# Kernel tuning notes

Measured on AMD Instinct MI355X. Metric: run time of the kernel, lower is better.

Reference implementation:

```python
import jax, jax.numpy as jnp
import numpy as np


def setup_inputs() -> dict:
    key = jax.random.key(0)
    x = jax.random.normal(key, (8192, 4096), dtype=jnp.float32)
    return {"x": x, "p": 64}


def reference(x, p):
    # training-mode path: find top-p indices per row (descending sort, first p)
    # and overwrite those positions with -1000. mask = ones, so mask*x == x.
    _, idx = jax.lax.top_k(x, p)                      # [B, p] int32
    rows = jnp.arange(x.shape[0])[:, None]            # [B, 1]
    out = x.at[rows, idx].set(jnp.float32(-1000.0))
    return out
```

## Files before the change

kernel.cpp:

```cpp
#include <hip/hip_runtime.h>
#include <stdint.h>

#define COLS 4096
#define NEGV (-1000.0f)

__device__ __forceinline__ uint32_t f2key(float f) {
    uint32_t u = __float_as_uint(f);
    return u ^ (uint32_t)(((int32_t)u >> 31) | (int32_t)0x80000000);
}
__device__ __forceinline__ float key2f(uint32_t k) {
    uint32_t u = (k & 0x80000000u) ? (k ^ 0x80000000u) : ~k;
    return __uint_as_float(u);
}

template <int PER>
__device__ __forceinline__ void find_bin(const uint32_t* hist, int t, int lane, int wave,
                                         uint32_t rem, uint32_t* s_wsum,
                                         volatile uint32_t* s_dig, volatile uint32_t* s_rem) {
    const int base = t * PER;
    uint32_t own[PER];
    uint32_t L = 0;
#pragma unroll
    for (int i = 0; i < PER; ++i) { own[i] = hist[base + i]; L += own[i]; }
    uint32_t inc = L;
#pragma unroll
    for (int d = 1; d < 64; d <<= 1) {
        uint32_t tmp = (uint32_t)__shfl_down((int)inc, d, 64);
        if (lane + d < 64) inc += tmp;
    }
    if (lane == 0) s_wsum[wave] = inc;
    __syncthreads();
    uint32_t U = inc - L;
#pragma unroll
    for (int w = 1; w < 4; ++w) if (wave + w < 4) U += s_wsum[wave + w];
    uint32_t acc = U;
#pragma unroll
    for (int i = PER - 1; i >= 0; --i) {
        uint32_t h = own[i];
        if (h != 0u && acc < rem && rem <= acc + h) {
            *s_dig = (uint32_t)(base + i);
            *s_rem = rem - acc;
        }
        acc += h;
    }
    __syncthreads();
}

extern "C" __global__ __launch_bounds__(256, 8)
void intent_dropout_kernel(const float* __restrict__ x,
                           const int* __restrict__ pp,
                           float* __restrict__ out) {
    __shared__ uint32_t s_h1[2048];
    __shared__ uint32_t s_h2[2048];
    __shared__ uint32_t s_grpmax[64];
    __shared__ uint32_t s_wsum[4];
    __shared__ uint32_t s_Ckey;
    __shared__ uint32_t s_dig, s_remv;
    __shared__ uint32_t s_eqcnt;

    const int row  = blockIdx.x;
    const int t    = threadIdx.x;
    const int lane = t & 63;
    const int wave = t >> 6;
    const uint32_t P = (uint32_t)pp[0];

    const float4* xr   = (const float4*)(x + (size_t)row * COLS);
    float4*       orow = (float4*)(out + (size_t)row * COLS);

    uint32_t keys[16];
#pragma unroll
    for (int j = 0; j < 4; ++j) {
        float4 v = xr[t + 256 * j];
        keys[4 * j + 0] = f2key(v.x);
        keys[4 * j + 1] = f2key(v.y);
        keys[4 * j + 2] = f2key(v.z);
        keys[4 * j + 3] = f2key(v.w);
    }
#pragma unroll
    for (int i = 0; i < 8; ++i) { s_h1[t + 256 * i] = 0u; s_h2[t + 256 * i] = 0u; }
    if (t == 0) s_eqcnt = 0u;

#pragma unroll
    for (int j = 0; j < 4; ++j) {
        uint32_t m = max(max(keys[4 * j], keys[4 * j + 1]), max(keys[4 * j + 2], keys[4 * j + 3]));
#pragma unroll
        for (int d = 1; d < 16; d <<= 1) m = max(m, (uint32_t)__shfl_xor((int)m, d, 64));
        if ((lane & 15) == 0) s_grpmax[(t >> 4) + 16 * j] = m;
    }
    __syncthreads();

    if (t < 64) {
        uint32_t g = s_grpmax[t];
#pragma unroll
        for (int d = 1; d < 64; d <<= 1) g = min(g, (uint32_t)__shfl_xor((int)g, d, 64));
        if (t == 0) s_Ckey = g;
    }
    __syncthreads();
    const uint32_t Ckey = s_Ckey;

#pragma unroll
    for (int i = 0; i < 16; ++i)
        if (keys[i] >= Ckey) atomicAdd(&s_h1[keys[i] >> 21], 1u);
    __syncthreads();
    find_bin<8>(s_h1, t, lane, wave, P, s_wsum, &s_dig, &s_remv);
    const uint32_t d1   = s_dig;
    const uint32_t rem1 = s_remv;

#pragma unroll
    for (int i = 0; i < 4; ++i) s_h1[t + 256 * i] = 0u;
#pragma unroll
    for (int i = 0; i < 16; ++i)
        if (keys[i] >= Ckey && (keys[i] >> 21) == d1)
            atomicAdd(&s_h2[(keys[i] >> 10) & 0x7FFu], 1u);
    __syncthreads();
    find_bin<8>(s_h2, t, lane, wave, rem1, s_wsum, &s_dig, &s_remv);
    const uint32_t d2   = s_dig;
    const uint32_t rem2 = s_remv;
    const uint32_t pre21 = (d1 << 11) | d2;

#pragma unroll
    for (int i = 0; i < 16; ++i)
        if (keys[i] >= Ckey && (keys[i] >> 10) == pre21)
            atomicAdd(&s_h1[keys[i] & 0x3FFu], 1u);
    __syncthreads();
    find_bin<4>(s_h1, t, lane, wave, rem2, s_wsum, &s_dig, &s_remv);
    const uint32_t Tkey = (pre21 << 10) | s_dig;
    const uint32_t keq  = s_remv;

#pragma unroll
    for (int j = 0; j < 4; ++j) {
#pragma unroll
        for (int c = 0; c < 4; ++c) {
            if (keys[4 * j + c] == Tkey) {
                uint32_t s = atomicAdd(&s_eqcnt, 1u);
                if (s < 2048u) s_h2[s] = (uint32_t)(4 * t + 1024 * j + c);
            }
        }
    }
    __syncthreads();
    const uint32_t eqc = (s_eqcnt < 2048u) ? s_eqcnt : 2048u;

#pragma unroll
    for (int j = 0; j < 4; ++j) {
        float4 o;
        float* comp = (float*)&o;
#pragma unroll
        for (int c = 0; c < 4; ++c) {
            uint32_t k = keys[4 * j + c];
            float f;
            if (k > Tkey) {
                f = NEGV;
            } else if (k == Tkey) {
                uint32_t myi = (uint32_t)(4 * t + 1024 * j + c);
                uint32_t r = 0;
                for (uint32_t e = 0; e < eqc; ++e) r += (uint32_t)(s_h2[e] < myi);
                f = (r < keq) ? NEGV : key2f(k);
            } else {
                f = key2f(k);
            }
            comp[c] = f;
        }
        orow[t + 256 * j] = o;
    }
}

extern "C" void kernel_launch(void* const* d_in, const int* in_sizes, int n_in,
                              void* d_out, int out_size, void* d_ws, size_t ws_size,
                              hipStream_t stream) {
    const float* x   = (const float*)d_in[0];
    const int*   pp  = (const int*)d_in[1];
    float*       out = (float*)d_out;
    int rows = in_sizes[0] / COLS;
    hipLaunchKernelGGL(intent_dropout_kernel, dim3(rows), dim3(256), 0, stream,
                       x, pp, out);
}
```

Baseline: 231.0 us.

## Replace later radix passes with small candidate-list rank selection and halve block size

Cuts the block to 128 threads, each holding 32 keys, which lowers LDS use (one histogram plus small candidate buffers) to allow more resident blocks. After the first 11-bit histogram pass, keys in the selected bin are compacted into a 128-entry candidate list and ranked by brute-force pairwise comparison to find the exact threshold key and cut index. The later radix passes run only when the list overflows, and exact ties fall back to an index histogram. This removes two histogram passes and the per-element tie-rank loop in the common case, at the cost of more register pressure and a more complex fallback path.

After: 261.9 us. +13.3%, slower.

```diff
diff --git a/kernel.cpp b/kernel.cpp
--- a/kernel.cpp
+++ b/kernel.cpp
@@ -2,6 +2,9 @@
 #include <stdint.h>
 
 #define COLS 4096
+#define TPB  128
+#define F4PT 8
+#define CAP  128
 #define NEGV (-1000.0f)
 
 __device__ __forceinline__ uint32_t f2key(float f) {
@@ -15,11 +18,10 @@
 
 template <int PER>
 __device__ __forceinline__ void find_bin(const uint32_t* hist, int t, int lane, int wave,
-                                         uint32_t rem, uint32_t* s_wsum,
+                                         uint32_t rem, volatile uint32_t* s_wsum,
                                          volatile uint32_t* s_dig, volatile uint32_t* s_rem) {
     const int base = t * PER;
-    uint32_t own[PER];
-    uint32_t L = 0;
+    uint32_t own[PER]; uint32_t L = 0;
 #pragma unroll
     for (int i = 0; i < PER; ++i) { own[i] = hist[base + i]; L += own[i]; }
     uint32_t inc = L;
@@ -31,32 +33,26 @@
     if (lane == 0) s_wsum[wave] = inc;
     __syncthreads();
     uint32_t U = inc - L;
-#pragma unroll
-    for (int w = 1; w < 4; ++w) if (wave + w < 4) U += s_wsum[wave + w];
+    if (wave == 0) U += s_wsum[1];
     uint32_t acc = U;
 #pragma unroll
     for (int i = PER - 1; i >= 0; --i) {
         uint32_t h = own[i];
-        if (h != 0u && acc < rem && rem <= acc + h) {
-            *s_dig = (uint32_t)(base + i);
-            *s_rem = rem - acc;
-        }
+        if (h && acc < rem && rem <= acc + h) { *s_dig = (uint32_t)(base + i); *s_rem = rem - acc; }
         acc += h;
     }
     __syncthreads();
 }
 
-extern "C" __global__ __launch_bounds__(256, 8)
+extern "C" __global__ __launch_bounds__(TPB, 8)
 void intent_dropout_kernel(const float* __restrict__ x,
                            const int* __restrict__ pp,
                            float* __restrict__ out) {
     __shared__ uint32_t s_h1[2048];
-    __shared__ uint32_t s_h2[2048];
+    __shared__ uint32_t s_ck[CAP], s_ci[CAP];
     __shared__ uint32_t s_grpmax[64];
-    __shared__ uint32_t s_wsum[4];
-    __shared__ uint32_t s_Ckey;
-    __shared__ uint32_t s_dig, s_remv;
-    __shared__ uint32_t s_eqcnt;
+    __shared__ uint32_t s_wsum[2];
+    __shared__ uint32_t s_Ckey, s_dig, s_remv, s_cnt, s_cnt2, s_Tkey, s_cutIdx, s_pbtie;
 
     const int row  = blockIdx.x;
     const int t    = threadIdx.x;
@@ -67,28 +63,22 @@
     const float4* xr   = (const float4*)(x + (size_t)row * COLS);
     float4*       orow = (float4*)(out + (size_t)row * COLS);
 
-    uint32_t keys[16];
-#pragma unroll
-    for (int j = 0; j < 4; ++j) {
-        float4 v = xr[t + 256 * j];
-        keys[4 * j + 0] = f2key(v.x);
-        keys[4 * j + 1] = f2key(v.y);
-        keys[4 * j + 2] = f2key(v.z);
-        keys[4 * j + 3] = f2key(v.w);
-    }
-#pragma unroll
-    for (int i = 0; i < 8; ++i) { s_h1[t + 256 * i] = 0u; s_h2[t + 256 * i] = 0u; }
-    if (t == 0) s_eqcnt = 0u;
-
-#pragma unroll
-    for (int j = 0; j < 4; ++j) {
-        uint32_t m = max(max(keys[4 * j], keys[4 * j + 1]), max(keys[4 * j + 2], keys[4 * j + 3]));
+#pragma unroll
+    for (int i = 0; i < 16; ++i) s_h1[t + TPB * i] = 0u;
+    if (t == 0) { s_cnt = 0u; s_cnt2 = 0u; }
+
+    uint32_t keys[32];
+#pragma unroll
+    for (int j = 0; j < F4PT; ++j) {
+        float4 v = xr[t + TPB * j];
+        keys[4*j+0] = f2key(v.x); keys[4*j+1] = f2key(v.y);
+        keys[4*j+2] = f2key(v.z); keys[4*j+3] = f2key(v.w);
+        uint32_t m = max(max(keys[4*j], keys[4*j+1]), max(keys[4*j+2], keys[4*j+3]));
 #pragma unroll
         for (int d = 1; d < 16; d <<= 1) m = max(m, (uint32_t)__shfl_xor((int)m, d, 64));
-        if ((lane & 15) == 0) s_grpmax[(t >> 4) + 16 * j] = m;
-    }
-    __syncthreads();
-
+        if ((lane & 15) == 0) s_grpmax[(t >> 4) + 8 * j] = m;
+    }
+    __syncthreads();
     if (t < 64) {
         uint32_t g = s_grpmax[t];
 #pragma unroll
@@ -99,68 +89,142 @@
     const uint32_t Ckey = s_Ckey;
 
 #pragma unroll
-    for (int i = 0; i < 16; ++i)
+    for (int i = 0; i < 32; ++i)
         if (keys[i] >= Ckey) atomicAdd(&s_h1[keys[i] >> 21], 1u);
     __syncthreads();
-    find_bin<8>(s_h1, t, lane, wave, P, s_wsum, &s_dig, &s_remv);
-    const uint32_t d1   = s_dig;
-    const uint32_t rem1 = s_remv;
-
-#pragma unroll
-    for (int i = 0; i < 4; ++i) s_h1[t + 256 * i] = 0u;
-#pragma unroll
-    for (int i = 0; i < 16; ++i)
-        if (keys[i] >= Ckey && (keys[i] >> 21) == d1)
-            atomicAdd(&s_h2[(keys[i] >> 10) & 0x7FFu], 1u);
-    __syncthreads();
-    find_bin<8>(s_h2, t, lane, wave, rem1, s_wsum, &s_dig, &s_remv);
-    const uint32_t d2   = s_dig;
-    const uint32_t rem2 = s_remv;
-    const uint32_t pre21 = (d1 << 11) | d2;
-
-#pragma unroll
-    for (int i = 0; i < 16; ++i)
-        if (keys[i] >= Ckey && (keys[i] >> 10) == pre21)
-            atomicAdd(&s_h1[keys[i] & 0x3FFu], 1u);
-    __syncthreads();
-    find_bin<4>(s_h1, t, lane, wave, rem2, s_wsum, &s_dig, &s_remv);
-    const uint32_t Tkey = (pre21 << 10) | s_dig;
-    const uint32_t keq  = s_remv;
-
-#pragma unroll
-    for (int j = 0; j < 4; ++j) {
+    find_bin<16>(s_h1, t, lane, wave, P, s_wsum, &s_dig, &s_remv);
+    const uint32_t d1 = s_dig, rem1 = s_remv;
+
+#pragma unroll
+    for (int j = 0; j < F4PT; ++j) {
 #pragma unroll
         for (int c = 0; c < 4; ++c) {
-            if (keys[4 * j + c] == Tkey) {
-                uint32_t s = atomicAdd(&s_eqcnt, 1u);
-                if (s < 2048u) s_h2[s] = (uint32_t)(4 * t + 1024 * j + c);
-            }
-        }
-    }
-    __syncthreads();
-    const uint32_t eqc = (s_eqcnt < 2048u) ? s_eqcnt : 2048u;
-
-#pragma unroll
-    for (int j = 0; j < 4; ++j) {
+            uint32_t k = keys[4*j+c];
+            if (k >= Ckey && (k >> 21) == d1) {
+                uint32_t s = atomicAdd(&s_cnt, 1u);
+                if (s < CAP) { s_ck[s] = k; s_ci[s] = (uint32_t)(4*(t + TPB*j) + c); }
+            }
+        }
+    }
+    __syncthreads();
+    const uint32_t cnt = s_cnt;
+
+    if (cnt <= CAP) {
+        if (t < 64) {
+            uint32_t ka = 0, ia = 0, kb = 0, ib = 0;
+            const bool ha = (uint32_t)t < cnt, hb = (uint32_t)(t + 64) < cnt;
+            if (ha) { ka = s_ck[t];      ia = s_ci[t]; }
+            if (hb) { kb = s_ck[t + 64]; ib = s_ci[t + 64]; }
+            uint32_t ra = 0, rb = 0;
+            for (uint32_t e = 0; e < cnt; ++e) {
+                uint32_t ke = s_ck[e], ie = s_ci[e];
+                ra += (uint32_t)((ke > ka) || (ke == ka && ie < ia));
+                rb += (uint32_t)((ke > kb) || (ke == kb && ie < ib));
+            }
+            if (ha && ra == rem1 - 1u) { s_Tkey = ka; s_cutIdx = ia; }
+            if (hb && rb == rem1 - 1u) { s_Tkey = kb; s_cutIdx = ib; }
+        }
+        __syncthreads();
+    } else {
+#pragma unroll
+        for (int i = 0; i < 16; ++i) s_h1[t + TPB * i] = 0u;
+        __syncthreads();
+#pragma unroll
+        for (int i = 0; i < 32; ++i) {
+            uint32_t k = keys[i];
+            if (k >= Ckey && (k >> 21) == d1) atomicAdd(&s_h1[(k >> 10) & 0x7FFu], 1u);
+        }
+        __syncthreads();
+        find_bin<16>(s_h1, t, lane, wave, rem1, s_wsum, &s_dig, &s_remv);
+        const uint32_t d2 = s_dig, rem2 = s_remv;
+        const uint32_t pre21 = (d1 << 11) | d2;
+#pragma unroll
+        for (int j = 0; j < F4PT; ++j) {
+#pragma unroll
+            for (int c = 0; c < 4; ++c) {
+                uint32_t k = keys[4*j+c];
+                if (k >= Ckey && (k >> 10) == pre21) {
+                    uint32_t s = atomicAdd(&s_cnt2, 1u);
+                    if (s < CAP) { s_ck[s] = k; s_ci[s] = (uint32_t)(4*(t + TPB*j) + c); }
+                }
+            }
+        }
+        __syncthreads();
+        const uint32_t cnt2 = s_cnt2;
+        if (cnt2 <= CAP) {
+            if (t < 64) {
+                uint32_t ka = 0, ia = 0, kb = 0, ib = 0;
+                const bool ha = (uint32_t)t < cnt2, hb = (uint32_t)(t + 64) < cnt2;
+                if (ha) { ka = s_ck[t];      ia = s_ci[t]; }
+                if (hb) { kb = s_ck[t + 64]; ib = s_ci[t + 64]; }
+                uint32_t ra = 0, rb = 0;
+                for (uint32_t e = 0; e < cnt2; ++e) {
+                    uint32_t ke = s_ck[e], ie = s_ci[e];
+                    ra += (uint32_t)((ke > ka) || (ke == ka && ie < ia));
+                    rb += (uint32_t)((ke > kb) || (ke == kb && ie < ib));
+                }
+                if (ha && ra == rem2 - 1u) { s_Tkey = ka; s_cutIdx = ia; }
+                if (hb && rb == rem2 - 1u) { s_Tkey = kb; s_cutIdx = ib; }
+            }
+            __syncthreads();
+        } else {
+#pragma unroll
+            for (int i = 0; i < 16; ++i) s_h1[t + TPB * i] = 0u;
+            __syncthreads();
+#pragma unroll
+            for (int i = 0; i < 32; ++i) {
+                uint32_t k = keys[i];
+                if (k >= Ckey && (k >> 10) == pre21) atomicAdd(&s_h1[k & 0x3FFu], 1u);
+            }
+            __syncthreads();
+            find_bin<8>(s_h1, t, lane, wave, rem2, s_wsum, &s_dig, &s_remv);
+            const uint32_t Tk  = (pre21 << 10) | s_dig;
+            const uint32_t keq = s_remv;
+#pragma unroll
+            for (int i = 0; i < 16; ++i) s_h1[t + TPB * i] = 0u;
+            __syncthreads();
+#pragma unroll
+            for (int j = 0; j < F4PT; ++j)
+#pragma unroll
+                for (int c = 0; c < 4; ++c)
+                    if (keys[4*j+c] == Tk)
+                        atomicAdd(&s_h1[2047u - ((uint32_t)(4*(t + TPB*j) + c) >> 1)], 1u);
+            __syncthreads();
+            find_bin<16>(s_h1, t, lane, wave, keq, s_wsum, &s_dig, &s_remv);
+            const uint32_t br = s_dig, remv = s_remv;
+            const uint32_t pairBase = 2u * (2047u - br);
+            {
+                const uint32_t f = pairBase >> 2;
+                if ((uint32_t)t == (f & (uint32_t)(TPB - 1))) {
+                    const uint32_t jj = f >> 7, cc = pairBase & 3u;
+                    s_pbtie = (uint32_t)(keys[4*jj + cc] == Tk);
+                }
+            }
+            __syncthreads();
+            if (t == 0) {
+                const uint32_t cp = s_h1[br];
+                uint32_t cut;
+                if (cp >= 2u) cut = (remv == 1u) ? pairBase : pairBase + 1u;
+                else          cut = s_pbtie ? pairBase : pairBase + 1u;
+                s_Tkey = Tk; s_cutIdx = cut;
+            }
+            __syncthreads();
+        }
+    }
+
+    const uint32_t Tkey = s_Tkey, cutIdx = s_cutIdx;
+#pragma unroll
+    for (int j = 0; j < F4PT; ++j) {
         float4 o;
-        float* comp = (float*)&o;
+        float* c4 = (float*)&o;
 #pragma unroll
         for (int c = 0; c < 4; ++c) {
-            uint32_t k = keys[4 * j + c];
-            float f;
-            if (k > Tkey) {
-                f = NEGV;
-            } else if (k == Tkey) {
-                uint32_t myi = (uint32_t)(4 * t + 1024 * j + c);
-                uint32_t r = 0;
-                for (uint32_t e = 0; e < eqc; ++e) r += (uint32_t)(s_h2[e] < myi);
-                f = (r < keq) ? NEGV : key2f(k);
-            } else {
-                f = key2f(k);
-            }
-            comp[c] = f;
-        }
-        orow[t + 256 * j] = o;
+            const uint32_t k   = keys[4*j+c];
+            const uint32_t idx = (uint32_t)(4*(t + TPB*j) + c);
+            const bool kill = (k > Tkey) || (k == Tkey && idx <= cutIdx);
+            c4[c] = kill ? NEGV : key2f(k);
+        }
+        orow[t + TPB * j] = o;
     }
 }
 
@@ -171,6 +235,6 @@
     const int*   pp  = (const int*)d_in[1];
     float*       out = (float*)d_out;
     int rows = in_sizes[0] / COLS;
-    hipLaunchKernelGGL(intent_dropout_kernel, dim3(rows), dim3(256), 0, stream,
+    hipLaunchKernelGGL(intent_dropout_kernel, dim3(rows), dim3(TPB), 0, stream,
                        x, pp, out);
 }
```

## Process each row with a single wavefront using compacted candidates and adaptive histogram

Applied to the files above, without the earlier changes.

Each row is now handled by one 64-lane wavefront that holds 64 keys per lane in registers, so block-wide barriers become wave shuffles. Candidates at or above the min-of-group-max threshold are compacted into shared memory as (key, inverted index) pairs. The cut is found with one adaptive 256-bin histogram over the candidate key range, then a small rank pass, with bitwise radix fallbacks when the candidate set is too large. This removes the three-pass 2048-bin histograms and the tie-handling loop, at the cost of heavy register use per lane and fewer threads per row.

After: 475.4 us. 2.06x slower.

```diff
diff --git a/kernel.cpp b/kernel.cpp
--- a/kernel.cpp
+++ b/kernel.cpp
@@ -2,165 +2,203 @@
 #include <stdint.h>
 
 #define COLS 4096
+#define CAP  512
 #define NEGV (-1000.0f)
 
-__device__ __forceinline__ uint32_t f2key(float f) {
-    uint32_t u = __float_as_uint(f);
+__device__ __forceinline__ uint32_t f2k(uint32_t u) {
     return u ^ (uint32_t)(((int32_t)u >> 31) | (int32_t)0x80000000);
 }
-__device__ __forceinline__ float key2f(uint32_t k) {
+__device__ __forceinline__ float k2f(uint32_t k) {
     uint32_t u = (k & 0x80000000u) ? (k ^ 0x80000000u) : ~k;
     return __uint_as_float(u);
 }
 
-template <int PER>
-__device__ __forceinline__ void find_bin(const uint32_t* hist, int t, int lane, int wave,
-                                         uint32_t rem, uint32_t* s_wsum,
-                                         volatile uint32_t* s_dig, volatile uint32_t* s_rem) {
-    const int base = t * PER;
-    uint32_t own[PER];
-    uint32_t L = 0;
-#pragma unroll
-    for (int i = 0; i < PER; ++i) { own[i] = hist[base + i]; L += own[i]; }
-    uint32_t inc = L;
-#pragma unroll
-    for (int d = 1; d < 64; d <<= 1) {
-        uint32_t tmp = (uint32_t)__shfl_down((int)inc, d, 64);
-        if (lane + d < 64) inc += tmp;
-    }
-    if (lane == 0) s_wsum[wave] = inc;
-    __syncthreads();
-    uint32_t U = inc - L;
-#pragma unroll
-    for (int w = 1; w < 4; ++w) if (wave + w < 4) U += s_wsum[wave + w];
-    uint32_t acc = U;
-#pragma unroll
-    for (int i = PER - 1; i >= 0; --i) {
-        uint32_t h = own[i];
-        if (h != 0u && acc < rem && rem <= acc + h) {
-            *s_dig = (uint32_t)(base + i);
-            *s_rem = rem - acc;
-        }
-        acc += h;
-    }
-    __syncthreads();
-}
-
-extern "C" __global__ __launch_bounds__(256, 8)
+extern "C" __global__ __launch_bounds__(64, 4)
 void intent_dropout_kernel(const float* __restrict__ x,
                            const int* __restrict__ pp,
                            float* __restrict__ out) {
-    __shared__ uint32_t s_h1[2048];
-    __shared__ uint32_t s_h2[2048];
-    __shared__ uint32_t s_grpmax[64];
-    __shared__ uint32_t s_wsum[4];
-    __shared__ uint32_t s_Ckey;
-    __shared__ uint32_t s_dig, s_remv;
-    __shared__ uint32_t s_eqcnt;
-
-    const int row  = blockIdx.x;
-    const int t    = threadIdx.x;
-    const int lane = t & 63;
-    const int wave = t >> 6;
+    __shared__ uint64_t s_pairs[CAP];
+    __shared__ uint32_t s_hist[256];
+    __shared__ uint64_t s_l2[64];
+
+    const int l   = threadIdx.x;
+    const int row = blockIdx.x;
     const uint32_t P = (uint32_t)pp[0];
 
-    const float4* xr   = (const float4*)(x + (size_t)row * COLS);
-    float4*       orow = (float4*)(out + (size_t)row * COLS);
-
-    uint32_t keys[16];
-#pragma unroll
-    for (int j = 0; j < 4; ++j) {
-        float4 v = xr[t + 256 * j];
-        keys[4 * j + 0] = f2key(v.x);
-        keys[4 * j + 1] = f2key(v.y);
-        keys[4 * j + 2] = f2key(v.z);
-        keys[4 * j + 3] = f2key(v.w);
-    }
-#pragma unroll
-    for (int i = 0; i < 8; ++i) { s_h1[t + 256 * i] = 0u; s_h2[t + 256 * i] = 0u; }
-    if (t == 0) s_eqcnt = 0u;
-
-#pragma unroll
-    for (int j = 0; j < 4; ++j) {
-        uint32_t m = max(max(keys[4 * j], keys[4 * j + 1]), max(keys[4 * j + 2], keys[4 * j + 3]));
-#pragma unroll
-        for (int d = 1; d < 16; d <<= 1) m = max(m, (uint32_t)__shfl_xor((int)m, d, 64));
-        if ((lane & 15) == 0) s_grpmax[(t >> 4) + 16 * j] = m;
-    }
-    __syncthreads();
-
-    if (t < 64) {
-        uint32_t g = s_grpmax[t];
-#pragma unroll
-        for (int d = 1; d < 64; d <<= 1) g = min(g, (uint32_t)__shfl_xor((int)g, d, 64));
-        if (t == 0) s_Ckey = g;
-    }
-    __syncthreads();
-    const uint32_t Ckey = s_Ckey;
-
-#pragma unroll
-    for (int i = 0; i < 16; ++i)
-        if (keys[i] >= Ckey) atomicAdd(&s_h1[keys[i] >> 21], 1u);
-    __syncthreads();
-    find_bin<8>(s_h1, t, lane, wave, P, s_wsum, &s_dig, &s_remv);
-    const uint32_t d1   = s_dig;
-    const uint32_t rem1 = s_remv;
-
-#pragma unroll
-    for (int i = 0; i < 4; ++i) s_h1[t + 256 * i] = 0u;
-#pragma unroll
-    for (int i = 0; i < 16; ++i)
-        if (keys[i] >= Ckey && (keys[i] >> 21) == d1)
-            atomicAdd(&s_h2[(keys[i] >> 10) & 0x7FFu], 1u);
-    __syncthreads();
-    find_bin<8>(s_h2, t, lane, wave, rem1, s_wsum, &s_dig, &s_remv);
-    const uint32_t d2   = s_dig;
-    const uint32_t rem2 = s_remv;
-    const uint32_t pre21 = (d1 << 11) | d2;
-
-#pragma unroll
-    for (int i = 0; i < 16; ++i)
-        if (keys[i] >= Ckey && (keys[i] >> 10) == pre21)
-            atomicAdd(&s_h1[keys[i] & 0x3FFu], 1u);
-    __syncthreads();
-    find_bin<4>(s_h1, t, lane, wave, rem2, s_wsum, &s_dig, &s_remv);
-    const uint32_t Tkey = (pre21 << 10) | s_dig;
-    const uint32_t keq  = s_remv;
-
-#pragma unroll
-    for (int j = 0; j < 4; ++j) {
-#pragma unroll
-        for (int c = 0; c < 4; ++c) {
-            if (keys[4 * j + c] == Tkey) {
-                uint32_t s = atomicAdd(&s_eqcnt, 1u);
-                if (s < 2048u) s_h2[s] = (uint32_t)(4 * t + 1024 * j + c);
-            }
-        }
-    }
-    __syncthreads();
-    const uint32_t eqc = (s_eqcnt < 2048u) ? s_eqcnt : 2048u;
-
-#pragma unroll
-    for (int j = 0; j < 4; ++j) {
+    const uint4* xr   = (const uint4*)(x + (size_t)row * COLS);
+    float4*      orow = (float4*)(out + (size_t)row * COLS);
+
+    s_hist[l] = 0u; s_hist[l + 64] = 0u; s_hist[l + 128] = 0u; s_hist[l + 192] = 0u;
+
+    uint32_t k[64];
+    uint32_t m = 0u;
+#pragma unroll
+    for (int q = 0; q < 16; ++q) {
+        uint4 u = xr[l + 64 * q];
+        uint32_t a = f2k(u.x), b = f2k(u.y), c = f2k(u.z), d = f2k(u.w);
+        k[4*q+0] = a; k[4*q+1] = b; k[4*q+2] = c; k[4*q+3] = d;
+        m = max(m, max(max(a, b), max(c, d)));
+    }
+    uint32_t Ck = m;
+#pragma unroll
+    for (int d = 1; d < 64; d <<= 1) Ck = min(Ck, (uint32_t)__shfl_xor((int)Ck, d));
+
+    uint32_t c = 0;
+#pragma unroll
+    for (int i = 0; i < 64; ++i) c += (uint32_t)(k[i] >= Ck);
+    uint32_t inc = c;
+#pragma unroll
+    for (int d = 1; d < 64; d <<= 1) {
+        uint32_t t = (uint32_t)__shfl_up((int)inc, d);
+        if (l >= d) inc += t;
+    }
+    const uint32_t M = (uint32_t)__shfl((int)inc, 63);
+    uint32_t off = inc - c;
+
+    uint64_t cutPair;
+
+    if (M <= CAP) {
+#pragma unroll
+        for (int q = 0; q < 16; ++q) {
+#pragma unroll
+            for (int cc = 0; cc < 4; ++cc) {
+                uint32_t kk = k[4*q+cc];
+                if (kk >= Ck) {
+                    uint32_t idx = (uint32_t)(4*l + 256*q + cc);
+                    s_pairs[off++] = ((uint64_t)kk << 32) | (uint32_t)(~idx);
+                }
+            }
+        }
+        __syncthreads();
+
+        uint64_t pr[8];
+        bool     va[8];
+#pragma unroll
+        for (int q = 0; q < 8; ++q) {
+            uint32_t slot = (uint32_t)l + 64u * q;
+            va[q] = slot < M;
+            pr[q] = va[q] ? s_pairs[slot] : 0ull;
+        }
+        uint32_t mnK = 0xFFFFFFFFu, mxK = 0u;
+#pragma unroll
+        for (int q = 0; q < 8; ++q)
+            if (va[q]) { uint32_t kk = (uint32_t)(pr[q] >> 32); mnK = min(mnK, kk); mxK = max(mxK, kk); }
+#pragma unroll
+        for (int d = 1; d < 64; d <<= 1) {
+            mnK = min(mnK, (uint32_t)__shfl_xor((int)mnK, d));
+            mxK = max(mxK, (uint32_t)__shfl_xor((int)mxK, d));
+        }
+        uint32_t dk = mnK ^ mxK;
+        int shift = 0;
+        if (dk) { int hb = 31 - __clz(dk); shift = hb > 7 ? hb - 7 : 0; }
+
+#pragma unroll
+        for (int q = 0; q < 8; ++q)
+            if (va[q]) atomicAdd(&s_hist[(((uint32_t)(pr[q] >> 32)) >> shift) & 255u], 1u);
+        __syncthreads();
+
+        uint32_t own0 = s_hist[4*l], own1 = s_hist[4*l+1], own2 = s_hist[4*l+2], own3 = s_hist[4*l+3];
+        uint32_t L = own0 + own1 + own2 + own3;
+        uint32_t sfx = L;
+#pragma unroll
+        for (int d = 1; d < 64; d <<= 1) {
+            uint32_t t = (uint32_t)__shfl_down((int)sfx, d);
+            if (l + d < 64) sfx += t;
+        }
+        uint32_t U = sfx - L;
+        uint32_t tb = 0, rb = 0; bool found = false;
+        {
+            uint32_t hh[4] = {own0, own1, own2, own3};
+            uint32_t acc = U;
+#pragma unroll
+            for (int i = 3; i >= 0; --i) {
+                uint32_t h = hh[i];
+                if (h && acc < P && P <= acc + h) { tb = (uint32_t)(4*l + i); rb = P - acc; found = true; }
+                acc += h;
+            }
+        }
+        unsigned long long fm = __ballot(found);
+        int src = (int)__builtin_ctzll(fm);
+        tb = (uint32_t)__shfl((int)tb, src);
+        rb = (uint32_t)__shfl((int)rb, src);
+
+        bool ib[8];
+        uint32_t c2 = 0;
+#pragma unroll
+        for (int q = 0; q < 8; ++q) {
+            ib[q] = va[q] && ((((uint32_t)(pr[q] >> 32)) >> shift) & 255u) == tb;
+            c2 += (uint32_t)ib[q];
+        }
+        uint32_t inc2 = c2;
+#pragma unroll
+        for (int d = 1; d < 64; d <<= 1) {
+            uint32_t t = (uint32_t)__shfl_up((int)inc2, d);
+            if (l >= d) inc2 += t;
+        }
+        const uint32_t n2 = (uint32_t)__shfl((int)inc2, 63);
+        uint32_t o2 = inc2 - c2;
+
+        if (n2 <= 64u) {
+#pragma unroll
+            for (int q = 0; q < 8; ++q)
+                if (ib[q]) s_l2[o2++] = pr[q];
+            __syncthreads();
+            uint64_t mine = (l < (int)n2) ? s_l2[l] : 0ull;
+            uint32_t r = 0;
+            for (uint32_t e = 0; e < n2; ++e) r += (uint32_t)(s_l2[e] > mine);
+            bool hit = (l < (int)n2) && (r == rb - 1u);
+            unsigned long long hm = __ballot(hit);
+            int hs = (int)__builtin_ctzll(hm);
+            cutPair = __shfl(mine, hs);
+        } else {
+            uint64_t prefix = 0ull; uint32_t rem = P;
+            for (int b = 63; b >= 0; --b) {
+                uint64_t candp = (prefix >> b) | 1ull;
+                uint32_t cnt = 0;
+#pragma unroll
+                for (int q = 0; q < 8; ++q)
+                    cnt += (uint32_t)(va[q] && (pr[q] >> b) == candp);
+#pragma unroll
+                for (int d = 1; d < 64; d <<= 1) cnt += (uint32_t)__shfl_xor((int)cnt, d);
+                if (cnt >= rem) prefix |= (1ull << b); else rem -= cnt;
+            }
+            cutPair = prefix;
+        }
+    } else {
+        uint64_t prefix = 0ull; uint32_t rem = P;
+        for (int b = 63; b >= 0; --b) {
+            uint64_t candp = (prefix >> b) | 1ull;
+            uint32_t cnt = 0;
+#pragma unroll
+            for (int q = 0; q < 16; ++q) {
+#pragma unroll
+                for (int cc = 0; cc < 4; ++cc) {
+                    uint32_t idx = (uint32_t)(4*l + 256*q + cc);
+                    uint64_t pv = ((uint64_t)k[4*q+cc] << 32) | (uint32_t)(~idx);
+                    cnt += (uint32_t)((pv >> b) == candp);
+                }
+            }
+#pragma unroll
+            for (int d = 1; d < 64; d <<= 1) cnt += (uint32_t)__shfl_xor((int)cnt, d);
+            if (cnt >= rem) prefix |= (1ull << b); else rem -= cnt;
+        }
+        cutPair = prefix;
+    }
+
+    const uint32_t Tkey = (uint32_t)(cutPair >> 32);
+    const uint32_t Tlow = (uint32_t)cutPair;
+#pragma unroll
+    for (int q = 0; q < 16; ++q) {
         float4 o;
-        float* comp = (float*)&o;
-#pragma unroll
-        for (int c = 0; c < 4; ++c) {
-            uint32_t k = keys[4 * j + c];
-            float f;
-            if (k > Tkey) {
-                f = NEGV;
-            } else if (k == Tkey) {
-                uint32_t myi = (uint32_t)(4 * t + 1024 * j + c);
-                uint32_t r = 0;
-                for (uint32_t e = 0; e < eqc; ++e) r += (uint32_t)(s_h2[e] < myi);
-                f = (r < keq) ? NEGV : key2f(k);
-            } else {
-                f = key2f(k);
-            }
-            comp[c] = f;
-        }
-        orow[t + 256 * j] = o;
+        float* c4 = (float*)&o;
+#pragma unroll
+        for (int cc = 0; cc < 4; ++cc) {
+            uint32_t kk = k[4*q+cc];
+            uint32_t ic = ~(uint32_t)(4*l + 256*q + cc);
+            bool kill = (kk > Tkey) || (kk == Tkey && ic >= Tlow);
+            c4[cc] = kill ? NEGV : k2f(kk);
+        }
+        orow[l + 64 * q] = o;
     }
 }
 
@@ -171,6 +209,6 @@
     const int*   pp  = (const int*)d_in[1];
     float*       out = (float*)d_out;
     int rows = in_sizes[0] / COLS;
-    hipLaunchKernelGGL(intent_dropout_kernel, dim3(rows), dim3(256), 0, stream,
+    hipLaunchKernelGGL(intent_dropout_kernel, dim3(rows), dim3(64), 0, stream,
                        x, pp, out);
 }
```
